# Kernel optimization log

Hardware: AMD Instinct MI355X
Metric: run time of the kernel (lower is better)

The kernel has to match this reference:

```python
import jax, jax.numpy as jnp
import numpy as np

D_IN, H1, H2, H3 = 1024, 512, 256, 128  # embedding MLP dims
D_CBP = 2048                             # compact bilinear pooling output dim
H_C = 1024                               # comparator hidden dim
CLASSES = 10
B = 16384
SLOPE = 0.2  # LeakyReLU negative slope


def _lrelu(x):
    return jnp.where(x >= 0, x, SLOPE * x)


def _embed(x, W1, b1, W2, b2, W3, b3):
    x = _lrelu(x @ W1 + b1)
    x = _lrelu(x @ W2 + b2)
    x = _lrelu(x @ W3 + b3)
    return x  # [B, 128]


def setup_inputs() -> dict:
    key = jax.random.key(0)
    ks = jax.random.split(key, 16)

    def lin(k, fan_in, fan_out):
        bound = 1.0 / np.sqrt(fan_in)
        kw, kb = jax.random.split(k)
        W = jax.random.uniform(kw, (fan_in, fan_out), jnp.float32, -bound, bound)
        b = jax.random.uniform(kb, (fan_out,), jnp.float32, -bound, bound)
        return W, b

    W1, b1 = lin(ks[0], D_IN, H1)
    W2, b2 = lin(ks[1], H1, H2)
    W3, b3 = lin(ks[2], H2, H3)
    Wc1, bc1 = lin(ks[3], D_CBP, H_C)
    Wc2, bc2 = lin(ks[4], H_C, CLASSES)

    X = jax.random.normal(ks[5], (B, D_IN), jnp.float32)
    Centers = jax.random.normal(ks[6], (B, D_IN), jnp.float32)

    # count-sketch hashes (int constants) and +-1 signs (float buffers)
    h1 = jax.random.randint(ks[7], (H3,), 0, D_CBP, jnp.int32)
    h2 = jax.random.randint(ks[8], (H3,), 0, D_CBP, jnp.int32)
    s1 = jnp.sign(jax.random.normal(ks[9], (H3,), jnp.float32)) + (jax.random.normal(ks[9], (H3,)) == 0)
    s2 = jnp.sign(jax.random.normal(ks[10], (H3,), jnp.float32)) + (jax.random.normal(ks[10], (H3,)) == 0)

    return {"X": X, "Centers": Centers,
            "W1": W1, "b1": b1, "W2": W2, "b2": b2, "W3": W3, "b3": b3,
            "h1": h1, "s1": s1, "h2": h2, "s2": s2,
            "Wc1": Wc1, "bc1": bc1, "Wc2": Wc2, "bc2": bc2}


def _cbp(x, y, h1, s1, h2, s2):
    # count-sketch via tiny dense sketch matrices [128, 2048]
    M1 = jnp.zeros((H3, D_CBP), x.dtype).at[jnp.arange(H3), h1].set(s1)
    M2 = jnp.zeros((H3, D_CBP), y.dtype).at[jnp.arange(H3), h2].set(s2)
    sk1 = x @ M1  # [B, 2048]
    sk2 = y @ M2
    # circular convolution via real FFT
    return jnp.fft.irfft(jnp.fft.rfft(sk1, axis=-1) * jnp.fft.rfft(sk2, axis=-1), n=D_CBP, axis=-1)


def reference(X, Centers, W1, b1, W2, b2, W3, b3, h1, s1, h2, s2, Wc1, bc1, Wc2, bc2):
    ex = _embed(X, W1, b1, W2, b2, W3, b3)        # [B, 128]
    ec = _embed(Centers, W1, b1, W2, b2, W3, b3)  # [B, 128]
    cbp = _cbp(ex, ec, h1, s1, h2, s2)            # [B, 2048]
    z = _lrelu(cbp @ Wc1 + bc1)                   # [B, 1024]
    logits = z @ Wc2 + bc2                        # [B, classes]
    return jax.nn.softmax(logits, axis=1)
```

## Files before the change

kernel.cpp:

```cpp
#include <hip/hip_runtime.h>
#include <hip/hip_bf16.h>
#include <math.h>

#define BATCH   16384
#define D_IN    1024
#define H1_DIM  512
#define H2_DIM  256
#define H3_DIM  128
#define D_CBP   2048
#define H_C     1024
#define CLASSES 10
#define SLOPE   0.2f

#define NK_PAD  1088
#define NF      (2 * NK_PAD)
#define NF_USED 2080

typedef short v8s __attribute__((ext_vector_type(8)));
typedef float v4f __attribute__((ext_vector_type(4)));
typedef unsigned short u16;
typedef unsigned int   u32;

__device__ __forceinline__ float b2f(unsigned short u) {
  return __uint_as_float(((unsigned)u) << 16);
}
__device__ __forceinline__ u16 f2b(float f) {
  __hip_bfloat16 h = __float2bfloat16(f);
  return __builtin_bit_cast(unsigned short, h);
}

__device__ __forceinline__ void g2l16(const void* g, void* l) {
  __builtin_amdgcn_global_load_lds(
      (const __attribute__((address_space(1))) void*)g,
      (__attribute__((address_space(3))) void*)l, 16, 0, 0);
}

__global__ __launch_bounds__(256) void gemm_bf16(
    const u16* __restrict__ A,
    const u16* __restrict__ Bt,
    const float* __restrict__ bias,
    u16* __restrict__ C,
    int M, int N, int K, int lda, int ldb, float slope)
{
  __shared__ __align__(16) short Asb[5][128 * 32];
  __shared__ __align__(16) short Bsb[5][128 * 32];

  const int tid  = threadIdx.x;
  const int wave = tid >> 6, lane = tid & 63;
  const int wm = wave >> 1, wn = wave & 1;
  const int u = lane & 15, quad = lane >> 4;

  const int nwg = gridDim.x * gridDim.y;
  int id = blockIdx.y * gridDim.x + blockIdx.x;
  if ((nwg & 7) == 0) id = (id & 7) * (nwg >> 3) + (id >> 3);
  const int m0 = (id / gridDim.x) * 128, n0 = (id % gridDim.x) * 128;

  const int g_log = ((lane & 3) - ((lane >> 3) & 3)) & 3;
  const int srow  = wave * 32 + (lane >> 2);
  const u16* gA0 = A  + (size_t)(m0 + srow)      * lda + g_log * 8;
  const u16* gA1 = A  + (size_t)(m0 + srow + 16) * lda + g_log * 8;
  const u16* gB0 = Bt + (size_t)(n0 + srow)      * ldb + g_log * 8;
  const u16* gB1 = Bt + (size_t)(n0 + srow + 16) * ldb + g_log * 8;
  const int lo0 = (wave * 32)      * 32;
  const int lo1 = (wave * 32 + 16) * 32;

  const int gran = (quad + (u >> 1)) & 3;
  int offA[4], offB[4];
#pragma unroll
  for (int i = 0; i < 4; ++i) {
    offA[i] = (wm * 64 + i * 16 + u) * 32 + gran * 8;
    offB[i] = (wn * 64 + i * 16 + u) * 32 + gran * 8;
  }

  v4f acc[4][4];
#pragma unroll
  for (int i = 0; i < 4; ++i)
#pragma unroll
    for (int j = 0; j < 4; ++j) acc[i][j] = (v4f){0.f, 0.f, 0.f, 0.f};

  const int nsteps = K >> 5;

  auto stage = [&](int s, int buf) {
    const int k0 = s * 32;
    g2l16(gA0 + k0, &Asb[buf][lo0]);
    g2l16(gA1 + k0, &Asb[buf][lo1]);
    g2l16(gB0 + k0, &Bsb[buf][lo0]);
    g2l16(gB1 + k0, &Bsb[buf][lo1]);
  };

  stage(0, 0);
  if (nsteps > 1) stage(1, 1);
  if (nsteps > 2) stage(2, 2);

  int cb = 0, sb = 3;
  for (int t = 0; t < nsteps; ++t) {
    if (t + 3 < nsteps) stage(t + 3, sb);

    const int rem = nsteps - 1 - t;
    if (rem >= 3)      asm volatile("s_waitcnt vmcnt(12)" ::: "memory");
    else if (rem == 2) asm volatile("s_waitcnt vmcnt(8)"  ::: "memory");
    else if (rem == 1) asm volatile("s_waitcnt vmcnt(4)"  ::: "memory");
    else               asm volatile("s_waitcnt vmcnt(0)"  ::: "memory");
    __builtin_amdgcn_s_barrier();
    asm volatile("" ::: "memory");

    v8s a[4], b[4];
#pragma unroll
    for (int i = 0; i < 4; ++i) a[i] = *(const v8s*)&Asb[cb][offA[i]];
#pragma unroll
    for (int j = 0; j < 4; ++j) b[j] = *(const v8s*)&Bsb[cb][offB[j]];
#pragma unroll
    for (int i = 0; i < 4; ++i)
#pragma unroll
      for (int j = 0; j < 4; ++j)
        acc[i][j] = __builtin_amdgcn_mfma_f32_16x16x32_bf16(a[i], b[j], acc[i][j], 0, 0, 0);

    cb = (cb == 4) ? 0 : cb + 1;
    sb = (sb == 4) ? 0 : sb + 1;
  }

  float bcol[4];
#pragma unroll
  for (int j = 0; j < 4; ++j) bcol[j] = bias[n0 + wn * 64 + j * 16 + u];
#pragma unroll
  for (int i = 0; i < 4; ++i)
#pragma unroll
    for (int r = 0; r < 4; ++r) {
      const size_t ro = (size_t)(m0 + wm * 64 + i * 16 + quad * 4 + r) * N
                        + n0 + wn * 64 + u;
#pragma unroll
      for (int j = 0; j < 4; ++j) {
        float v = acc[i][j][r] + bcol[j];
        v = v >= 0.f ? v : slope * v;
        C[ro + j * 16] = f2b(v);
      }
    }
}

__device__ __forceinline__ void f_pass(
    const u16* gA0, const u16* gA1, const u16* gB0, const u16* gB1,
    short (*Asb)[128 * 32], short (*Bsb)[128 * 32],
    int lo0, int lo1, const int* offA, const int* offB,
    v4f (&acc)[4][4])
{
  auto stage = [&](int s, int buf) {
    const int k0 = s * 32;
    g2l16(gA0 + k0, &Asb[buf][lo0]);
    g2l16(gA1 + k0, &Asb[buf][lo1]);
    g2l16(gB0 + k0, &Bsb[buf][lo0]);
    g2l16(gB1 + k0, &Bsb[buf][lo1]);
  };
  stage(0, 0); stage(1, 1); stage(2, 2);
#pragma unroll
  for (int t = 0; t < 4; ++t) {
    if (t == 0) stage(3, 3);
    if (t == 0)      asm volatile("s_waitcnt vmcnt(12)" ::: "memory");
    else if (t == 1) asm volatile("s_waitcnt vmcnt(8)"  ::: "memory");
    else if (t == 2) asm volatile("s_waitcnt vmcnt(4)"  ::: "memory");
    else             asm volatile("s_waitcnt vmcnt(0)"  ::: "memory");
    __builtin_amdgcn_s_barrier();
    asm volatile("" ::: "memory");
    v8s a[4], b[4];
#pragma unroll
    for (int i = 0; i < 4; ++i) a[i] = *(const v8s*)&Asb[t][offA[i]];
#pragma unroll
    for (int j = 0; j < 4; ++j) b[j] = *(const v8s*)&Bsb[t][offB[j]];
#pragma unroll
    for (int i = 0; i < 4; ++i)
#pragma unroll
      for (int j = 0; j < 4; ++j)
        acc[i][j] = __builtin_amdgcn_mfma_f32_16x16x32_bf16(a[i], b[j], acc[i][j], 0, 0, 0);
  }
}

__global__ __launch_bounds__(256) void gemm_f1f2(
    const u16* __restrict__ E3,
    const u16* __restrict__ C1t,
    const u16* __restrict__ C2t,
    u16* __restrict__ F1)
{
  __shared__ __align__(16) short Asb[5][128 * 32];
  __shared__ __align__(16) short Bsb[5][128 * 32];

  const int tid  = threadIdx.x;
  const int wave = tid >> 6, lane = tid & 63;
  const int wm = wave >> 1, wn = wave & 1;
  const int u = lane & 15, quad = lane >> 4;
  const int N = NF, K = H3_DIM;

  const int nwg = gridDim.x * gridDim.y;
  int id = blockIdx.y * gridDim.x + blockIdx.x;
  if ((nwg & 7) == 0) id = (id & 7) * (nwg >> 3) + (id >> 3);
  const int m0 = (id / gridDim.x) * 128, n0 = (id % gridDim.x) * 128;

  const int g_log = ((lane & 3) - ((lane >> 3) & 3)) & 3;
  const int srow  = wave * 32 + (lane >> 2);
  const size_t aoffX = (size_t)(m0 + srow) * K + g_log * 8;
  const size_t boff  = (size_t)(n0 + srow) * K + g_log * 8;
  const int lo0 = (wave * 32)      * 32;
  const int lo1 = (wave * 32 + 16) * 32;

  const int gran = (quad + (u >> 1)) & 3;
  int offA[4], offB[4];
#pragma unroll
  for (int i = 0; i < 4; ++i) {
    offA[i] = (wm * 64 + i * 16 + u) * 32 + gran * 8;
    offB[i] = (wn * 64 + i * 16 + u) * 32 + gran * 8;
  }

  v4f acc1[4][4], acc2[4][4];
#pragma unroll
  for (int i = 0; i < 4; ++i)
#pragma unroll
    for (int j = 0; j < 4; ++j) {
      acc1[i][j] = (v4f){0.f, 0.f, 0.f, 0.f};
      acc2[i][j] = (v4f){0.f, 0.f, 0.f, 0.f};
    }

  f_pass(E3 + aoffX, E3 + aoffX + (size_t)16 * K,
         C1t + boff, C1t + boff + (size_t)16 * K,
         Asb, Bsb, lo0, lo1, offA, offB, acc1);
  const size_t aoffC = aoffX + (size_t)BATCH * K;
  f_pass(E3 + aoffC, E3 + aoffC + (size_t)16 * K,
         C2t + boff, C2t + boff + (size_t)16 * K,
         Asb, Bsb, lo0, lo1, offA, offB, acc2);

  const bool im = (u & 1);
#pragma unroll
  for (int i = 0; i < 4; ++i)
#pragma unroll
    for (int r = 0; r < 4; ++r) {
      const size_t ro = (size_t)(m0 + wm * 64 + i * 16 + quad * 4 + r) * N
                        + n0 + wn * 64 + u;
#pragma unroll
      for (int j = 0; j < 4; ++j) {
        const float f1v = acc1[i][j][r];
        const float f1p = __shfl_xor(f1v, 1, 64);
        const float f2v = acc2[i][j][r];
        const float f2p = __shfl_xor(f2v, 1, 64);
        const float outv = im ? (f1p * f2v + f1v * f2p)
                              : (f1v * f2v - f1p * f2p);
        F1[ro + j * 16] = f2b(outv);
      }
    }
}

#define CAST_NB (BATCH * D_IN / 4 / 256)
__global__ __launch_bounds__(256) void cast2_bf16(
    const float* __restrict__ srcA, const float* __restrict__ srcB,
    u16* __restrict__ dst)
{
  const int bx = blockIdx.x;
  const float* s = (bx < CAST_NB) ? srcA : srcB;
  const int i = ((bx < CAST_NB) ? bx : bx - CAST_NB) * 256 + threadIdx.x;
  u16* d = dst + ((bx < CAST_NB) ? 0 : (size_t)BATCH * D_IN);
  const float4 v = ((const float4*)s)[i];
  __align__(8) u16 o[4] = {f2b(v.x), f2b(v.y), f2b(v.z), f2b(v.w)};
  *(uint2*)(d + (size_t)i * 4) = *(uint2*)o;
}

__global__ __launch_bounds__(256) void transpose_cast4(
    const float* __restrict__ W1, u16* __restrict__ W1t,
    const float* __restrict__ W2, u16* __restrict__ W2t,
    const float* __restrict__ W3, u16* __restrict__ W3t,
    const float* __restrict__ Wc1, u16* __restrict__ Wc1t)
{
  __shared__ float tile[32][33];
  const int z = blockIdx.z;
  const float* W; u16* Wt; int K, N;
  if      (z == 0) { W = W1;  Wt = W1t;  K = D_IN;   N = H1_DIM; }
  else if (z == 1) { W = W2;  Wt = W2t;  K = H1_DIM; N = H2_DIM; }
  else if (z == 2) { W = W3;  Wt = W3t;  K = H2_DIM; N = H3_DIM; }
  else             { W = Wc1; Wt = Wc1t; K = D_CBP;  N = H_C;    }
  const int k0 = blockIdx.x * 32, n0 = blockIdx.y * 32;
  if (k0 >= K || n0 >= N) return;
  const int tx = threadIdx.x & 31, ty = threadIdx.x >> 5;
#pragma unroll
  for (int s = 0; s < 4; ++s) {
    const int k = ty * 4 + s;
    tile[k][tx] = W[(size_t)(k0 + k) * N + n0 + tx];
  }
  __syncthreads();
#pragma unroll
  for (int s = 0; s < 4; ++s) {
    const int n = ty * 4 + s;
    Wt[(size_t)(n0 + n) * K + k0 + tx] = f2b(tile[tx][n]);
  }
}


__global__ __launch_bounds__(256) void setup_tab(
    float2* __restrict__ tab, float* __restrict__ zbias)
{
  const int t = blockIdx.x * 256 + threadIdx.x;
  if (t < D_CBP) {
    const float ang = 6.2831853071795864769f * (float)t / (float)D_CBP;
    tab[t] = make_float2(__cosf(ang), __sinf(ang));
  }
  if (t < NF) zbias[t] = 0.f;
}

__global__ __launch_bounds__(256) void gen_C(
    const float2* __restrict__ tab,
    const int* __restrict__ h1, const float* __restrict__ s1,
    const int* __restrict__ h2, const float* __restrict__ s2,
    u16* __restrict__ C1t, u16* __restrict__ C2t)
{
  const int id = blockIdx.x * 256 + threadIdx.x;
  if (id >= NF * H3_DIM) return;
  const int m = id >> 7, i = id & 127;
  const int k = m >> 1;
  float v1 = 0.f, v2 = 0.f;
  if (m < 2 * (D_CBP / 2 + 1)) {
    const float2 c1 = tab[(k * h1[i]) & (D_CBP - 1)];
    const float2 c2 = tab[(k * h2[i]) & (D_CBP - 1)];
    v1 = (m & 1) ? -s1[i] * c1.y : s1[i] * c1.x;
    v2 = (m & 1) ? -s2[i] * c2.y : s2[i] * c2.x;
  }
  C1t[id] = f2b(v1);
  C2t[id] = f2b(v2);
}

__global__ __launch_bounds__(256) void gen_T(
    const float2* __restrict__ tab, u16* __restrict__ Tt)
{
  const int id = blockIdx.x * 256 + threadIdx.x;
  const int m = id >> 8, q0 = (id & 255) * 8;
  const int k = m >> 1;
  const float sc = ((k == 0) || (k == D_CBP / 2)) ? (1.f / D_CBP) : (2.f / D_CBP);
  __align__(16) u16 o[8];
#pragma unroll
  for (int j = 0; j < 8; ++j) {
    float v = 0.f;
    if (m < 2 * (D_CBP / 2 + 1)) {
      const float2 cs = tab[(k * (q0 + j)) & (D_CBP - 1)];
      v = (m & 1) ? -sc * cs.y : sc * cs.x;
    }
    o[j] = f2b(v);
  }
  *(v8s*)&Tt[(size_t)m * D_CBP + q0] = *(v8s*)o;
}

__global__ __launch_bounds__(256) void head_softmax(
    const u16* __restrict__ Z, const float* __restrict__ Wc2,
    const float* __restrict__ bc2, float* __restrict__ out)
{
  const int row  = blockIdx.x * 4 + (threadIdx.x >> 6);
  const int lane = threadIdx.x & 63;

  float acc[CLASSES];
#pragma unroll
  for (int c = 0; c < CLASSES; ++c) acc[c] = 0.f;

  const u16* z = Z + (size_t)row * H_C;
  for (int k = lane; k < H_C; k += 64) {
    const float zv = b2f(z[k]);
    const float* w = Wc2 + (size_t)k * CLASSES;
#pragma unroll
    for (int c = 0; c < CLASSES; ++c) acc[c] += zv * w[c];
  }
#pragma unroll
  for (int c = 0; c < CLASSES; ++c) {
#pragma unroll
    for (int off = 32; off > 0; off >>= 1)
      acc[c] += __shfl_down(acc[c], off);
  }
  if (lane == 0) {
    float l[CLASSES], mx = -1e30f;
#pragma unroll
    for (int c = 0; c < CLASSES; ++c) { l[c] = acc[c] + bc2[c]; mx = fmaxf(mx, l[c]); }
    float s = 0.f;
#pragma unroll
    for (int c = 0; c < CLASSES; ++c) { l[c] = __expf(l[c] - mx); s += l[c]; }
    const float inv = 1.f / s;
#pragma unroll
    for (int c = 0; c < CLASSES; ++c) out[(size_t)row * CLASSES + c] = l[c] * inv;
  }
}

extern "C" void kernel_launch(void* const* d_in, const int* in_sizes, int n_in,
                              void* d_out, int out_size, void* d_ws, size_t ws_size,
                              hipStream_t stream) {
  const float* X       = (const float*)d_in[0];
  const float* Centers = (const float*)d_in[1];
  const float* W1      = (const float*)d_in[2];
  const float* b1      = (const float*)d_in[3];
  const float* W2      = (const float*)d_in[4];
  const float* b2      = (const float*)d_in[5];
  const float* W3      = (const float*)d_in[6];
  const float* b3      = (const float*)d_in[7];
  const int*   h1      = (const int*)d_in[8];
  const float* s1      = (const float*)d_in[9];
  const int*   h2      = (const int*)d_in[10];
  const float* s2      = (const float*)d_in[11];
  const float* Wc1     = (const float*)d_in[12];
  const float* bc1     = (const float*)d_in[13];
  const float* Wc2     = (const float*)d_in[14];
  const float* bc2     = (const float*)d_in[15];
  float* out = (float*)d_out;

  char* ws = (char*)d_ws;
  const size_t MB = 1u << 20;
  const size_t KB = 1u << 10;
  u16*    Xb    = (u16*)(ws);
  u16*    Tt    = (u16*)(ws);
  u16*    FWt   = (u16*)(ws + 8 * MB + 512 * KB);
  u16*    F1    = (u16*)(ws + 13 * MB);
  u16*    E1b   = (u16*)(ws + 64 * MB);
  u16*    Zb    = (u16*)(ws + 81 * MB);
  u16*    E2b   = (u16*)(ws + 96 * MB);
  u16*    E3b   = (u16*)(ws + 113 * MB);
  u16*    W1t   = (u16*)(ws + 121 * MB);
  u16*    W2t   = (u16*)(ws + 122 * MB);
  u16*    W3t   = (u16*)(ws + 122 * MB + 256 * KB);
  u16*    Wc1t  = (u16*)(ws + 122 * MB + 512 * KB);
  u16*    C1t   = (u16*)(ws + 126 * MB + 512 * KB);
  u16*    C2t   = (u16*)(ws + 127 * MB + 64 * KB);
  float2* tab   = (float2*)(ws + 127 * MB + 640 * KB);
  float*  zbias = (float*)(ws + 127 * MB + 672 * KB);

  const dim3 blk(256);

  cast2_bf16<<<dim3(2 * CAST_NB), blk, 0, stream>>>(X, Centers, Xb);

  transpose_cast4<<<dim3(D_CBP / 32, H_C / 32, 4), blk, 0, stream>>>(
      W1, W1t, W2, W2t, W3, W3t, Wc1, Wc1t);

  setup_tab<<<dim3(9), blk, 0, stream>>>(tab, zbias);
  gen_C<<<dim3(NF * H3_DIM / 256), blk, 0, stream>>>(tab, h1, s1, h2, s2, C1t, C2t);

  gemm_bf16<<<dim3(H1_DIM / 128, 2 * BATCH / 128), blk, 0, stream>>>(
      Xb, W1t, b1, E1b, 2 * BATCH, H1_DIM, D_IN, D_IN, D_IN, SLOPE);

  gen_T<<<dim3(NF), blk, 0, stream>>>(tab, Tt);
  gemm_bf16<<<dim3(NF / 128, H_C / 128), blk, 0, stream>>>(
      Wc1t, Tt, zbias, FWt, H_C, NF, D_CBP, D_CBP, D_CBP, 1.0f);

  gemm_bf16<<<dim3(H2_DIM / 128, 2 * BATCH / 128), blk, 0, stream>>>(
      E1b, W2t, b2, E2b, 2 * BATCH, H2_DIM, H1_DIM, H1_DIM, H1_DIM, SLOPE);
  gemm_bf16<<<dim3(H3_DIM / 128, 2 * BATCH / 128), blk, 0, stream>>>(
      E2b, W3t, b3, E3b, 2 * BATCH, H3_DIM, H2_DIM, H2_DIM, H2_DIM, SLOPE);

  gemm_f1f2<<<dim3(NF / 128, BATCH / 128), blk, 0, stream>>>(
      E3b, C1t, C2t, F1);

  gemm_bf16<<<dim3(H_C / 128, BATCH / 128), blk, 0, stream>>>(
      F1, FWt, bc1, Zb, BATCH, H_C, NF_USED, NF, NF, SLOPE);

  head_softmax<<<dim3(BATCH / 4), blk, 0, stream>>>(Zb, Wc2, bc2, out);
}
```

Before: 470.2 us.

## Merge all preprocessing kernels into one launch and raise MFMA wave priority

Folds the input cast, the four weight transposes, the twiddle table, C/T generation and the zero-bias setup into a single prep kernel that dispatches on block index. The twiddle table is dropped and cos/sin are computed inline, and Tt moves to a separate workspace region so it no longer aliases Xb. It also wraps the MFMA blocks in s_setprio to favour matrix issue. The aim is to cut launch count and serialization between small kernels, at the cost of extra transcendental work in the generators and an unbalanced mixed-work grid.

New measurement: 453.6 us. 1.04x faster.

```diff
diff --git a/kernel.cpp b/kernel.cpp
--- a/kernel.cpp
+++ b/kernel.cpp
@@ -29,6 +29,11 @@
   return __builtin_bit_cast(unsigned short, h);
 }
 
+__device__ __forceinline__ float2 twiddle(int idx) {
+  const float ang = 6.2831853071795864769f * (float)idx / 2048.f;
+  return make_float2(__cosf(ang), __sinf(ang));
+}
+
 __device__ __forceinline__ void g2l16(const void* g, void* l) {
   __builtin_amdgcn_global_load_lds(
       (const __attribute__((address_space(1))) void*)g,
@@ -109,11 +114,13 @@
     for (int i = 0; i < 4; ++i) a[i] = *(const v8s*)&Asb[cb][offA[i]];
 #pragma unroll
     for (int j = 0; j < 4; ++j) b[j] = *(const v8s*)&Bsb[cb][offB[j]];
+    __builtin_amdgcn_s_setprio(1);
 #pragma unroll
     for (int i = 0; i < 4; ++i)
 #pragma unroll
       for (int j = 0; j < 4; ++j)
         acc[i][j] = __builtin_amdgcn_mfma_f32_16x16x32_bf16(a[i], b[j], acc[i][j], 0, 0, 0);
+    __builtin_amdgcn_s_setprio(0);
 
     cb = (cb == 4) ? 0 : cb + 1;
     sb = (sb == 4) ? 0 : sb + 1;
@@ -165,11 +172,13 @@
     for (int i = 0; i < 4; ++i) a[i] = *(const v8s*)&Asb[t][offA[i]];
 #pragma unroll
     for (int j = 0; j < 4; ++j) b[j] = *(const v8s*)&Bsb[t][offB[j]];
+    __builtin_amdgcn_s_setprio(1);
 #pragma unroll
     for (int i = 0; i < 4; ++i)
 #pragma unroll
       for (int j = 0; j < 4; ++j)
         acc[i][j] = __builtin_amdgcn_mfma_f32_16x16x32_bf16(a[i], b[j], acc[i][j], 0, 0, 0);
+    __builtin_amdgcn_s_setprio(0);
   }
 }
 
@@ -245,100 +254,115 @@
     }
 }
 
-#define CAST_NB (BATCH * D_IN / 4 / 256)
-__global__ __launch_bounds__(256) void cast2_bf16(
-    const float* __restrict__ srcA, const float* __restrict__ srcB,
-    u16* __restrict__ dst)
-{
-  const int bx = blockIdx.x;
-  const float* s = (bx < CAST_NB) ? srcA : srcB;
-  const int i = ((bx < CAST_NB) ? bx : bx - CAST_NB) * 256 + threadIdx.x;
-  u16* d = dst + ((bx < CAST_NB) ? 0 : (size_t)BATCH * D_IN);
-  const float4 v = ((const float4*)s)[i];
-  __align__(8) u16 o[4] = {f2b(v.x), f2b(v.y), f2b(v.z), f2b(v.w)};
-  *(uint2*)(d + (size_t)i * 4) = *(uint2*)o;
-}
-
-__global__ __launch_bounds__(256) void transpose_cast4(
+#define CAST_NB   (BATCH * D_IN / 4 / 256)
+#define NB_CAST   (2 * CAST_NB)
+#define NB_TW1    ((D_IN / 32) * (H1_DIM / 32))
+#define NB_TW2    ((H1_DIM / 32) * (H2_DIM / 32))
+#define NB_TW3    ((H2_DIM / 32) * (H3_DIM / 32))
+#define NB_TWC1   ((D_CBP / 32) * (H_C / 32))
+#define NB_TRANS  (NB_TW1 + NB_TW2 + NB_TW3 + NB_TWC1)
+#define NB_GENC   (NF * H3_DIM / 256)
+#define NB_GENT   (NF)
+#define NB_ZB     9
+#define NB_PREP   (NB_CAST + NB_TRANS + NB_GENC + NB_GENT + NB_ZB)
+
+__global__ __launch_bounds__(256) void prep_all(
+    const float* __restrict__ X, const float* __restrict__ Centers,
+    u16* __restrict__ Xb,
     const float* __restrict__ W1, u16* __restrict__ W1t,
     const float* __restrict__ W2, u16* __restrict__ W2t,
     const float* __restrict__ W3, u16* __restrict__ W3t,
-    const float* __restrict__ Wc1, u16* __restrict__ Wc1t)
+    const float* __restrict__ Wc1, u16* __restrict__ Wc1t,
+    const int* __restrict__ h1, const float* __restrict__ s1,
+    const int* __restrict__ h2, const float* __restrict__ s2,
+    u16* __restrict__ C1t, u16* __restrict__ C2t,
+    u16* __restrict__ Tt, float* __restrict__ zbias)
 {
   __shared__ float tile[32][33];
-  const int z = blockIdx.z;
-  const float* W; u16* Wt; int K, N;
-  if      (z == 0) { W = W1;  Wt = W1t;  K = D_IN;   N = H1_DIM; }
-  else if (z == 1) { W = W2;  Wt = W2t;  K = H1_DIM; N = H2_DIM; }
-  else if (z == 2) { W = W3;  Wt = W3t;  K = H2_DIM; N = H3_DIM; }
-  else             { W = Wc1; Wt = Wc1t; K = D_CBP;  N = H_C;    }
-  const int k0 = blockIdx.x * 32, n0 = blockIdx.y * 32;
-  if (k0 >= K || n0 >= N) return;
-  const int tx = threadIdx.x & 31, ty = threadIdx.x >> 5;
-#pragma unroll
-  for (int s = 0; s < 4; ++s) {
-    const int k = ty * 4 + s;
-    tile[k][tx] = W[(size_t)(k0 + k) * N + n0 + tx];
-  }
-  __syncthreads();
-#pragma unroll
-  for (int s = 0; s < 4; ++s) {
-    const int n = ty * 4 + s;
-    Wt[(size_t)(n0 + n) * K + k0 + tx] = f2b(tile[tx][n]);
-  }
-}
-
-
-__global__ __launch_bounds__(256) void setup_tab(
-    float2* __restrict__ tab, float* __restrict__ zbias)
-{
-  const int t = blockIdx.x * 256 + threadIdx.x;
-  if (t < D_CBP) {
-    const float ang = 6.2831853071795864769f * (float)t / (float)D_CBP;
-    tab[t] = make_float2(__cosf(ang), __sinf(ang));
-  }
-  if (t < NF) zbias[t] = 0.f;
-}
-
-__global__ __launch_bounds__(256) void gen_C(
-    const float2* __restrict__ tab,
-    const int* __restrict__ h1, const float* __restrict__ s1,
-    const int* __restrict__ h2, const float* __restrict__ s2,
-    u16* __restrict__ C1t, u16* __restrict__ C2t)
-{
-  const int id = blockIdx.x * 256 + threadIdx.x;
-  if (id >= NF * H3_DIM) return;
-  const int m = id >> 7, i = id & 127;
-  const int k = m >> 1;
-  float v1 = 0.f, v2 = 0.f;
-  if (m < 2 * (D_CBP / 2 + 1)) {
-    const float2 c1 = tab[(k * h1[i]) & (D_CBP - 1)];
-    const float2 c2 = tab[(k * h2[i]) & (D_CBP - 1)];
-    v1 = (m & 1) ? -s1[i] * c1.y : s1[i] * c1.x;
-    v2 = (m & 1) ? -s2[i] * c2.y : s2[i] * c2.x;
-  }
-  C1t[id] = f2b(v1);
-  C2t[id] = f2b(v2);
-}
-
-__global__ __launch_bounds__(256) void gen_T(
-    const float2* __restrict__ tab, u16* __restrict__ Tt)
-{
-  const int id = blockIdx.x * 256 + threadIdx.x;
-  const int m = id >> 8, q0 = (id & 255) * 8;
-  const int k = m >> 1;
-  const float sc = ((k == 0) || (k == D_CBP / 2)) ? (1.f / D_CBP) : (2.f / D_CBP);
-  __align__(16) u16 o[8];
-#pragma unroll
-  for (int j = 0; j < 8; ++j) {
-    float v = 0.f;
+  int bx = blockIdx.x;
+  const int t = threadIdx.x;
+
+  if (bx < NB_CAST) {
+    const float* s = (bx < CAST_NB) ? X : Centers;
+    const int i = ((bx < CAST_NB) ? bx : bx - CAST_NB) * 256 + t;
+    u16* d = Xb + ((bx < CAST_NB) ? 0 : (size_t)BATCH * D_IN);
+    const float4 v = ((const float4*)s)[i];
+    __align__(8) u16 o[4] = {f2b(v.x), f2b(v.y), f2b(v.z), f2b(v.w)};
+    *(uint2*)(d + (size_t)i * 4) = *(uint2*)o;
+    return;
+  }
+  bx -= NB_CAST;
+
+  if (bx < NB_TRANS) {
+    const float* W; u16* Wt; int K, N;
+    if (bx < NB_TW1)        { W = W1;  Wt = W1t;  K = D_IN;   N = H1_DIM; }
+    else if (bx < NB_TW1 + NB_TW2) {
+      bx -= NB_TW1;           W = W2;  Wt = W2t;  K = H1_DIM; N = H2_DIM; }
+    else if (bx < NB_TW1 + NB_TW2 + NB_TW3) {
+      bx -= NB_TW1 + NB_TW2;  W = W3;  Wt = W3t;  K = H2_DIM; N = H3_DIM; }
+    else {
+      bx -= NB_TW1 + NB_TW2 + NB_TW3;
+                              W = Wc1; Wt = Wc1t; K = D_CBP;  N = H_C;    }
+    const int nt = N / 32;
+    const int k0 = (bx / nt) * 32, n0 = (bx % nt) * 32;
+    const int tx = t & 31, ty = t >> 5;
+#pragma unroll
+    for (int s = 0; s < 4; ++s) {
+      const int k = ty * 4 + s;
+      tile[k][tx] = W[(size_t)(k0 + k) * N + n0 + tx];
+    }
+    __syncthreads();
+#pragma unroll
+    for (int s = 0; s < 4; ++s) {
+      const int n = ty * 4 + s;
+      Wt[(size_t)(n0 + n) * K + k0 + tx] = f2b(tile[tx][n]);
+    }
+    return;
+  }
+  bx -= NB_TRANS;
+
+  if (bx < NB_GENC) {
+    const int id = bx * 256 + t;
+    const int m = id >> 7, i = id & 127;
+    const int k = m >> 1;
+    float v1 = 0.f, v2 = 0.f;
     if (m < 2 * (D_CBP / 2 + 1)) {
-      const float2 cs = tab[(k * (q0 + j)) & (D_CBP - 1)];
-      v = (m & 1) ? -sc * cs.y : sc * cs.x;
-    }
-    o[j] = f2b(v);
-  }
-  *(v8s*)&Tt[(size_t)m * D_CBP + q0] = *(v8s*)o;
+      const float2 c1 = twiddle((k * h1[i]) & (D_CBP - 1));
+      const float2 c2 = twiddle((k * h2[i]) & (D_CBP - 1));
+      v1 = (m & 1) ? -s1[i] * c1.y : s1[i] * c1.x;
+      v2 = (m & 1) ? -s2[i] * c2.y : s2[i] * c2.x;
+    }
+    C1t[id] = f2b(v1);
+    C2t[id] = f2b(v2);
+    return;
+  }
+  bx -= NB_GENC;
+
+  if (bx < NB_GENT) {
+    const int id = bx * 256 + t;
+    const int m = id >> 8, q0 = (id & 255) * 8;
+    const int k = m >> 1;
+    const float sc = ((k == 0) || (k == D_CBP / 2)) ? (1.f / D_CBP)
+                                                    : (2.f / D_CBP);
+    __align__(16) u16 o[8];
+#pragma unroll
+    for (int j = 0; j < 8; ++j) {
+      float v = 0.f;
+      if (m < 2 * (D_CBP / 2 + 1)) {
+        const float2 cs = twiddle((k * (q0 + j)) & (D_CBP - 1));
+        v = (m & 1) ? -sc * cs.y : sc * cs.x;
+      }
+      o[j] = f2b(v);
+    }
+    *(v8s*)&Tt[(size_t)m * D_CBP + q0] = *(v8s*)o;
+    return;
+  }
+  bx -= NB_GENT;
+
+  {
+    const int i = bx * 256 + t;
+    if (i < NF) zbias[i] = 0.f;
+  }
 }
 
 __global__ __launch_bounds__(256) void head_softmax(
@@ -403,12 +427,12 @@
   const size_t MB = 1u << 20;
   const size_t KB = 1u << 10;
   u16*    Xb    = (u16*)(ws);
-  u16*    Tt    = (u16*)(ws);
   u16*    FWt   = (u16*)(ws + 8 * MB + 512 * KB);
   u16*    F1    = (u16*)(ws + 13 * MB);
   u16*    E1b   = (u16*)(ws + 64 * MB);
   u16*    Zb    = (u16*)(ws + 81 * MB);
   u16*    E2b   = (u16*)(ws + 96 * MB);
+  u16*    Tt    = (u16*)(ws + 96 * MB);
   u16*    E3b   = (u16*)(ws + 113 * MB);
   u16*    W1t   = (u16*)(ws + 121 * MB);
   u16*    W2t   = (u16*)(ws + 122 * MB);
@@ -416,23 +440,17 @@
   u16*    Wc1t  = (u16*)(ws + 122 * MB + 512 * KB);
   u16*    C1t   = (u16*)(ws + 126 * MB + 512 * KB);
   u16*    C2t   = (u16*)(ws + 127 * MB + 64 * KB);
-  float2* tab   = (float2*)(ws + 127 * MB + 640 * KB);
   float*  zbias = (float*)(ws + 127 * MB + 672 * KB);
 
   const dim3 blk(256);
 
-  cast2_bf16<<<dim3(2 * CAST_NB), blk, 0, stream>>>(X, Centers, Xb);
-
-  transpose_cast4<<<dim3(D_CBP / 32, H_C / 32, 4), blk, 0, stream>>>(
-      W1, W1t, W2, W2t, W3, W3t, Wc1, Wc1t);
-
-  setup_tab<<<dim3(9), blk, 0, stream>>>(tab, zbias);
-  gen_C<<<dim3(NF * H3_DIM / 256), blk, 0, stream>>>(tab, h1, s1, h2, s2, C1t, C2t);
+  prep_all<<<dim3(NB_PREP), blk, 0, stream>>>(
+      X, Centers, Xb, W1, W1t, W2, W2t, W3, W3t, Wc1, Wc1t,
+      h1, s1, h2, s2, C1t, C2t, Tt, zbias);
 
   gemm_bf16<<<dim3(H1_DIM / 128, 2 * BATCH / 128), blk, 0, stream>>>(
       Xb, W1t, b1, E1b, 2 * BATCH, H1_DIM, D_IN, D_IN, D_IN, SLOPE);
 
-  gen_T<<<dim3(NF), blk, 0, stream>>>(tab, Tt);
   gemm_bf16<<<dim3(NF / 128, H_C / 128), blk, 0, stream>>>(
       Wc1t, Tt, zbias, FWt, H_C, NF, D_CBP, D_CBP, D_CBP, 1.0f);
 
```
